# Kernel tuning notes

Measured on AMD Instinct MI355X. Metric: run time of the kernel, lower is better.

Reference implementation:

```python
import jax, jax.numpy as jnp
import numpy as np

EPS = 1e-12
FINAL_GROUPS = 256  # 4*64
FINAL_BIAS = 8.0


def resilu(x):
    # ReSiLU at default hardness == soft sigmoid gate
    return jax.nn.sigmoid(x)


def popcnt_layer(x, sel, w, b):
    # x: [B, In], sel: [O, P] int, w: [O, P], b: [O]
    selected = jnp.take(x, sel, axis=1)          # [B, O, P] gather
    weighted = selected * resilu(w)[None, :, :]  # weighted multiply
    summed = weighted.sum(axis=-1)               # [B, O] segment sum
    return resilu(summed - b[None, :])


def layer_norm(x, g, b):
    mu = x.mean(axis=-1, keepdims=True)
    var = ((x - mu) ** 2).mean(axis=-1, keepdims=True)
    return (x - mu) * jax.lax.rsqrt(var + EPS) * g + b


def setup_inputs() -> dict:
    key = jax.random.key(0)
    ks = jax.random.split(key, 16)
    B, IN, O1, O3, P = 256, 3200, 8192, 4096, 128
    return {
        "x": jax.random.normal(ks[0], (B, IN), dtype=jnp.float32),
        "sel1": jax.random.randint(ks[1], (O1, P), 0, IN, dtype=jnp.int32),
        "w1": jax.random.normal(ks[2], (O1, P), dtype=jnp.float32),
        "b1": jax.random.normal(ks[3], (O1,), dtype=jnp.float32) * (P / 3) + (P / 4),
        "g1": jnp.ones((O1,), dtype=jnp.float32),
        "be1": jnp.zeros((O1,), dtype=jnp.float32),
        "sel2": jax.random.randint(ks[4], (O1, P), 0, O1, dtype=jnp.int32),
        "w2": jax.random.normal(ks[5], (O1, P), dtype=jnp.float32),
        "b2": jax.random.normal(ks[6], (O1,), dtype=jnp.float32) * (P / 3) + (P / 4),
        "g2": jnp.ones((O1,), dtype=jnp.float32),
        "be2": jnp.zeros((O1,), dtype=jnp.float32),
        "sel3": jax.random.randint(ks[7], (O3, P), 0, O1, dtype=jnp.int32),
        "w3": jax.random.normal(ks[8], (O3, P), dtype=jnp.float32),
        "b3": jax.random.normal(ks[9], (O3,), dtype=jnp.float32) * (P / 3) + (P / 4),
    }


def reference(x, sel1, w1, b1, g1, be1, sel2, w2, b2, g2, be2, sel3, w3, b3):
    h = popcnt_layer(x, sel1, w1, b1)
    h = layer_norm(h, g1, be1)
    h = popcnt_layer(h, sel2, w2, b2)
    h = layer_norm(h, g2, be2)
    h = popcnt_layer(h, sel3, w3, b3)          # [B, 4096]
    out = h.reshape(h.shape[0], FINAL_GROUPS, -1).sum(axis=-1) - FINAL_BIAS  # [B, 256]
    return out
```

## Files before the change

kernel.cpp:

```cpp
#include <hip/hip_runtime.h>
#include <hip/hip_fp16.h>
#include <stdint.h>

#define BATCH 256
#define PSEL  128
#define IN_DIM 3200
#define O1_DIM 8192
#define O3_DIM 4096

__global__ __launch_bounds__(256) void transpose_kernel(const float* __restrict__ x,
                                                        __half* __restrict__ xT,
                                                        float* __restrict__ stats) {
    int tx = threadIdx.x;
    int ty = threadIdx.y;
    int tid = ty * 32 + tx;
    int gid = blockIdx.y * gridDim.x + blockIdx.x;
    if (gid < 4) stats[gid * 256 + tid] = 0.0f;

    __shared__ float tile[32][33];
    int i0 = blockIdx.x * 32;
    int b0 = blockIdx.y * 32;
#pragma unroll
    for (int k = 0; k < 4; ++k)
        tile[ty + k * 8][tx] =
            __builtin_nontemporal_load(&x[(size_t)(b0 + ty + k * 8) * IN_DIM + i0 + tx]);
    __syncthreads();
#pragma unroll
    for (int k = 0; k < 4; ++k)
        xT[(size_t)(i0 + ty + k * 8) * BATCH + b0 + tx] =
            __float2half(tile[tx][ty + k * 8]);
}

__global__ __launch_bounds__(256) void stats_kernel(const __half* __restrict__ hT,
                                                    float* __restrict__ gsum,
                                                    float* __restrict__ gsq) {
    int t   = threadIdx.x;
    int col = t & 127;
    int rp  = t >> 7;
    int r0  = blockIdx.x * 128 + rp * 64;
    const uint32_t* p = (const uint32_t*)hT + (size_t)r0 * 128 + col;
    float s0 = 0.f, s1 = 0.f, q0 = 0.f, q1 = 0.f;
#pragma unroll
    for (int ob = 0; ob < 8; ++ob) {
        uint32_t d[8];
#pragma unroll
        for (int j = 0; j < 8; ++j) d[j] = p[(size_t)(ob * 8 + j) * 128];
#pragma unroll
        for (int j = 0; j < 8; ++j) {
            float2 f = __half22float2(*(const __half2*)&d[j]);
            s0 += f.x; q0 = fmaf(f.x, f.x, q0);
            s1 += f.y; q1 = fmaf(f.y, f.y, q1);
        }
    }
    __shared__ float4 s_red[128];
    if (rp == 1) s_red[col] = make_float4(s0, s1, q0, q1);
    __syncthreads();
    if (rp == 0) {
        float4 r = s_red[col];
        atomicAdd(&gsum[2 * col],     s0 + r.x);
        atomicAdd(&gsum[2 * col + 1], s1 + r.y);
        atomicAdd(&gsq[2 * col],      q0 + r.z);
        atomicAdd(&gsq[2 * col + 1],  q1 + r.w);
    }
}

template <bool NORM>
__global__ __launch_bounds__(256, 4) void popcnt_kernel(
    const __half* __restrict__ actT,
    const int* __restrict__ sel,
    const float* __restrict__ w,
    const float* __restrict__ bias,
    const float* __restrict__ g,
    const float* __restrict__ be,
    const float* __restrict__ gsum,
    const float* __restrict__ gsq,
    float inv_n,
    __half* __restrict__ outp)
{
    const int o  = blockIdx.x;
    const int t  = threadIdx.x;
    const int cw = t & 31;
    const int rg = t >> 5;

    __shared__ uint32_t s_off[PSEL];
    __shared__ float    s_A[PSEL];
    __shared__ float s_rA[PSEL], s_rC[PSEL];
    __shared__ float s_acc[8][264];
    __shared__ float s_sums[2];

    if (t < PSEL) {
        int idx  = __builtin_nontemporal_load(&sel[o * PSEL + t]);
        float ww = __builtin_nontemporal_load(&w[o * PSEL + t]);
        float sw = 1.0f / (1.0f + __expf(-ww));
        float a, c;
        if (NORM) { a = sw * g[idx]; c = sw * be[idx]; }
        else      { a = sw;          c = 0.0f; }
        s_off[t] = (uint32_t)idx << 9;
        s_A[t]   = a;
        if (NORM) { s_rA[t] = a; s_rC[t] = c; }
    }
    __syncthreads();

    if (NORM && t < 64) {
        float va = s_rA[t] + s_rA[t + 64];
        float vc = s_rC[t] + s_rC[t + 64];
#pragma unroll
        for (int off = 32; off > 0; off >>= 1) {
            va += __shfl_down(va, off, 64);
            vc += __shfl_down(vc, off, 64);
        }
        if (t == 0) { s_sums[0] = va; s_sums[1] = vc; }
    }

    const uint32_t lane_off = (uint32_t)(cw << 4);
    uint32_t voff[16];
#pragma unroll
    for (int j = 0; j < 16; ++j)
        voff[j] = s_off[j * 8 + rg] + lane_off;
    uint4 d[16];
#pragma unroll
    for (int j = 0; j < 16; ++j)
        asm volatile("global_load_dwordx4 %0, %1, %2 sc0"
                     : "=v"(d[j])
                     : "v"(voff[j]), "s"(actT)
                     : "memory");
    asm volatile("s_waitcnt vmcnt(0)" ::: "memory");
    __builtin_amdgcn_sched_barrier(0);

    float acc[8] = {0.f, 0.f, 0.f, 0.f, 0.f, 0.f, 0.f, 0.f};
#pragma unroll
    for (int j = 0; j < 16; ++j) {
        float A = s_A[j * 8 + rg];
        const __half2* hp = (const __half2*)&d[j];
        float2 f0 = __half22float2(hp[0]);
        float2 f1 = __half22float2(hp[1]);
        float2 f2 = __half22float2(hp[2]);
        float2 f3 = __half22float2(hp[3]);
        acc[0] = fmaf(A, f0.x, acc[0]);
        acc[1] = fmaf(A, f0.y, acc[1]);
        acc[2] = fmaf(A, f1.x, acc[2]);
        acc[3] = fmaf(A, f1.y, acc[3]);
        acc[4] = fmaf(A, f2.x, acc[4]);
        acc[5] = fmaf(A, f2.y, acc[5]);
        acc[6] = fmaf(A, f3.x, acc[6]);
        acc[7] = fmaf(A, f3.y, acc[7]);
    }

    *(float4*)&s_acc[rg][8 * cw]     = make_float4(acc[0], acc[1], acc[2], acc[3]);
    *(float4*)&s_acc[rg][8 * cw + 4] = make_float4(acc[4], acc[5], acc[6], acc[7]);
    __syncthreads();

    float ab = 0.0f;
#pragma unroll
    for (int r = 0; r < 8; ++r) ab += s_acc[r][t];

    float bo = bias[o];
    float z;
    if (NORM) {
        float m  = gsum[t] * inv_n;
        float q  = gsq[t] * inv_n;
        float rs = rsqrtf(q - m * m + 1e-12f);
        z = rs * ab + s_sums[1] - rs * m * s_sums[0] - bo;
    } else {
        z = ab - bo;
    }
    float h = 1.0f / (1.0f + __expf(-z));
    __builtin_nontemporal_store(__half_as_ushort(__float2half(h)),
                                (unsigned short*)outp + (size_t)o * BATCH + t);
}

__global__ __launch_bounds__(256) void final_reduce(const __half* __restrict__ h3T,
                                                    float* __restrict__ out) {
    int gidx = blockIdx.x;
    int b    = threadIdx.x;
    const unsigned short* p = (const unsigned short*)h3T + (size_t)gidx * 16 * BATCH + b;
    float s = -8.0f;
#pragma unroll
    for (int j = 0; j < 16; ++j)
        s += __half2float(__ushort_as_half(__builtin_nontemporal_load(p + j * BATCH)));
    __builtin_nontemporal_store(s, &out[(size_t)b * 256 + gidx]);
}

extern "C" void kernel_launch(void* const* d_in, const int* in_sizes, int n_in,
                              void* d_out, int out_size, void* d_ws, size_t ws_size,
                              hipStream_t stream) {
    const float* x    = (const float*)d_in[0];
    const int*   sel1 = (const int*)d_in[1];
    const float* w1   = (const float*)d_in[2];
    const float* b1   = (const float*)d_in[3];
    const float* g1   = (const float*)d_in[4];
    const float* be1  = (const float*)d_in[5];
    const int*   sel2 = (const int*)d_in[6];
    const float* w2   = (const float*)d_in[7];
    const float* b2   = (const float*)d_in[8];
    const float* g2   = (const float*)d_in[9];
    const float* be2  = (const float*)d_in[10];
    const int*   sel3 = (const int*)d_in[11];
    const float* w3   = (const float*)d_in[12];
    const float* b3   = (const float*)d_in[13];
    float* out = (float*)d_out;

    char* ws = (char*)d_ws;
    __half* xT  = (__half*)(ws);
    __half* h1T = (__half*)(ws + 1638400);
    __half* h2T = (__half*)(ws + 1638400 + 4194304);
    __half* h3T = h1T;
    float* stats = (float*)(ws + 1638400 + 2 * 4194304);
    float* gs1 = stats;
    float* gq1 = stats + 256;
    float* gs2 = stats + 512;
    float* gq2 = stats + 768;

    transpose_kernel<<<dim3(IN_DIM / 32, BATCH / 32), dim3(32, 8), 0, stream>>>(
        x, xT, stats);

    popcnt_kernel<false><<<O1_DIM, 256, 0, stream>>>(
        xT, sel1, w1, b1, nullptr, nullptr, nullptr, nullptr, 0.0f, h1T);

    stats_kernel<<<O1_DIM / 128, 256, 0, stream>>>(h1T, gs1, gq1);

    popcnt_kernel<true><<<O1_DIM, 256, 0, stream>>>(
        h1T, sel2, w2, b2, g1, be1, gs1, gq1, 1.0f / (float)O1_DIM, h2T);

    stats_kernel<<<O1_DIM / 128, 256, 0, stream>>>(h2T, gs2, gq2);

    popcnt_kernel<true><<<O3_DIM, 256, 0, stream>>>(
        h2T, sel3, w3, b3, g2, be2, gs2, gq2, 1.0f / (float)O1_DIM, h3T);

    final_reduce<<<256, 256, 0, stream>>>(h3T, out);
}
```

Before: 181.6 us.

## Process several outputs per block with software-pipelined gather prefetch

Each popcnt block now handles 8 (or 4) consecutive outputs instead of one. The gather loads, sel and w for the next output are issued while the current output is reduced and stored, using double-buffered shared offsets and weights. Per-batch normalization factors are computed once per block. This aims to hide gather latency and cut per-block launch and setup overhead, but grid parallelism drops and the hand-written waitcnt counts make the schedule fragile.

```diff
diff --git a/kernel.cpp b/kernel.cpp
--- a/kernel.cpp
+++ b/kernel.cpp
@@ -75,98 +75,171 @@
     const float* __restrict__ gsum,
     const float* __restrict__ gsq,
     float inv_n,
-    __half* __restrict__ outp)
+    __half* __restrict__ outp,
+    int nout)
 {
-    const int o  = blockIdx.x;
     const int t  = threadIdx.x;
     const int cw = t & 31;
     const int rg = t >> 5;
-
-    __shared__ uint32_t s_off[PSEL];
-    __shared__ float    s_A[PSEL];
-    __shared__ float s_rA[PSEL], s_rC[PSEL];
-    __shared__ float s_acc[8][264];
-    __shared__ float s_sums[2];
+    const int o0 = blockIdx.x * nout;
+
+    __shared__ uint32_t s_off[2][PSEL];
+    __shared__ float    s_A[2][PSEL];
+    __shared__ float    s_part[2][4];
+    __shared__ float    s_acc[8][264];
+
+    const uint32_t lane_off = (uint32_t)(cw << 4);
+
+    float rs = 0.0f, rsm = 0.0f;
+    if (NORM) {
+        float m = gsum[t] * inv_n;
+        float q = gsq[t] * inv_n;
+        rs  = rsqrtf(q - m * m + 1e-12f);
+        rsm = rs * m;
+    }
 
     if (t < PSEL) {
-        int idx  = __builtin_nontemporal_load(&sel[o * PSEL + t]);
-        float ww = __builtin_nontemporal_load(&w[o * PSEL + t]);
-        float sw = 1.0f / (1.0f + __expf(-ww));
+        int   sv = sel[(size_t)o0 * PSEL + t];
+        float wv = w[(size_t)o0 * PSEL + t];
+        float sw = 1.0f / (1.0f + __expf(-wv));
         float a, c;
-        if (NORM) { a = sw * g[idx]; c = sw * be[idx]; }
-        else      { a = sw;          c = 0.0f; }
-        s_off[t] = (uint32_t)idx << 9;
-        s_A[t]   = a;
-        if (NORM) { s_rA[t] = a; s_rC[t] = c; }
+        if (NORM) { a = sw * g[sv]; c = sw * be[sv]; }
+        else      { a = sw;         c = 0.0f; }
+        s_off[0][t] = (uint32_t)sv << 9;
+        s_A[0][t]   = a;
+        if (NORM) {
+            float va = a, vc = c;
+#pragma unroll
+            for (int off = 32; off > 0; off >>= 1) {
+                va += __shfl_down(va, off, 64);
+                vc += __shfl_down(vc, off, 64);
+            }
+            if ((t & 63) == 0) {
+                s_part[0][(t >> 6) * 2 + 0] = va;
+                s_part[0][(t >> 6) * 2 + 1] = vc;
+            }
+        }
     }
     __syncthreads();
 
-    if (NORM && t < 64) {
-        float va = s_rA[t] + s_rA[t + 64];
-        float vc = s_rC[t] + s_rC[t + 64];
-#pragma unroll
-        for (int off = 32; off > 0; off >>= 1) {
-            va += __shfl_down(va, off, 64);
-            vc += __shfl_down(vc, off, 64);
-        }
-        if (t == 0) { s_sums[0] = va; s_sums[1] = vc; }
-    }
-
-    const uint32_t lane_off = (uint32_t)(cw << 4);
-    uint32_t voff[16];
-#pragma unroll
-    for (int j = 0; j < 16; ++j)
-        voff[j] = s_off[j * 8 + rg] + lane_off;
+    uint32_t raw_sel = 0, raw_w = 0;
+    if (nout > 1 && t < PSEL) {
+        const int*   sp = sel + (size_t)(o0 + 1) * PSEL;
+        const float* wp = w   + (size_t)(o0 + 1) * PSEL;
+        uint32_t vo = (uint32_t)(t * 4);
+        asm volatile("global_load_dword %0, %1, %2 nt" : "=v"(raw_sel) : "v"(vo), "s"(sp) : "memory");
+        asm volatile("global_load_dword %0, %1, %2 nt" : "=v"(raw_w)   : "v"(vo), "s"(wp) : "memory");
+    }
     uint4 d[16];
-#pragma unroll
-    for (int j = 0; j < 16; ++j)
-        asm volatile("global_load_dwordx4 %0, %1, %2 sc0"
-                     : "=v"(d[j])
-                     : "v"(voff[j]), "s"(actT)
-                     : "memory");
-    asm volatile("s_waitcnt vmcnt(0)" ::: "memory");
-    __builtin_amdgcn_sched_barrier(0);
-
-    float acc[8] = {0.f, 0.f, 0.f, 0.f, 0.f, 0.f, 0.f, 0.f};
-#pragma unroll
-    for (int j = 0; j < 16; ++j) {
-        float A = s_A[j * 8 + rg];
-        const __half2* hp = (const __half2*)&d[j];
-        float2 f0 = __half22float2(hp[0]);
-        float2 f1 = __half22float2(hp[1]);
-        float2 f2 = __half22float2(hp[2]);
-        float2 f3 = __half22float2(hp[3]);
-        acc[0] = fmaf(A, f0.x, acc[0]);
-        acc[1] = fmaf(A, f0.y, acc[1]);
-        acc[2] = fmaf(A, f1.x, acc[2]);
-        acc[3] = fmaf(A, f1.y, acc[3]);
-        acc[4] = fmaf(A, f2.x, acc[4]);
-        acc[5] = fmaf(A, f2.y, acc[5]);
-        acc[6] = fmaf(A, f3.x, acc[6]);
-        acc[7] = fmaf(A, f3.y, acc[7]);
-    }
-
-    *(float4*)&s_acc[rg][8 * cw]     = make_float4(acc[0], acc[1], acc[2], acc[3]);
-    *(float4*)&s_acc[rg][8 * cw + 4] = make_float4(acc[4], acc[5], acc[6], acc[7]);
-    __syncthreads();
-
-    float ab = 0.0f;
-#pragma unroll
-    for (int r = 0; r < 8; ++r) ab += s_acc[r][t];
-
-    float bo = bias[o];
-    float z;
-    if (NORM) {
-        float m  = gsum[t] * inv_n;
-        float q  = gsq[t] * inv_n;
-        float rs = rsqrtf(q - m * m + 1e-12f);
-        z = rs * ab + s_sums[1] - rs * m * s_sums[0] - bo;
-    } else {
-        z = ab - bo;
-    }
-    float h = 1.0f / (1.0f + __expf(-z));
-    __builtin_nontemporal_store(__half_as_ushort(__float2half(h)),
-                                (unsigned short*)outp + (size_t)o * BATCH + t);
+    {
+        uint32_t voff[16];
+#pragma unroll
+        for (int j = 0; j < 16; ++j) voff[j] = s_off[0][j * 8 + rg] + lane_off;
+#pragma unroll
+        for (int j = 0; j < 16; ++j)
+            asm volatile("global_load_dwordx4 %0, %1, %2 sc0"
+                         : "=v"(d[j]) : "v"(voff[j]), "s"(actT) : "memory");
+    }
+
+    for (int i = 0; i < nout; ++i) {
+        const int cur = i & 1, nxt = cur ^ 1;
+        const bool havenext = (i + 1 < nout);
+
+        float sw_n = 0.0f; int sv_n = 0;
+        uint32_t gv_u = 0, bv_u = 0;
+        if (havenext && t < PSEL) {
+            asm volatile("s_waitcnt vmcnt(16)" ::: "memory");
+            __builtin_amdgcn_sched_barrier(0);
+            sv_n = (int)raw_sel;
+            float wv = __uint_as_float(raw_w);
+            sw_n = 1.0f / (1.0f + __expf(-wv));
+            if (NORM) {
+                uint32_t vo = (uint32_t)(sv_n * 4);
+                asm volatile("global_load_dword %0, %1, %2" : "=v"(gv_u) : "v"(vo), "s"(g)  : "memory");
+                asm volatile("global_load_dword %0, %1, %2" : "=v"(bv_u) : "v"(vo), "s"(be) : "memory");
+            }
+        }
+
+        asm volatile("s_waitcnt vmcnt(0)" ::: "memory");
+        __builtin_amdgcn_sched_barrier(0);
+        if (havenext && t < PSEL) {
+            float a, c;
+            if (NORM) { a = sw_n * __uint_as_float(gv_u); c = sw_n * __uint_as_float(bv_u); }
+            else      { a = sw_n;                         c = 0.0f; }
+            s_off[nxt][t] = (uint32_t)sv_n << 9;
+            s_A[nxt][t]   = a;
+            if (NORM) {
+                float va = a, vc = c;
+#pragma unroll
+                for (int off = 32; off > 0; off >>= 1) {
+                    va += __shfl_down(va, off, 64);
+                    vc += __shfl_down(vc, off, 64);
+                }
+                if ((t & 63) == 0) {
+                    s_part[nxt][(t >> 6) * 2 + 0] = va;
+                    s_part[nxt][(t >> 6) * 2 + 1] = vc;
+                }
+            }
+        }
+        float acc[8] = {0.f, 0.f, 0.f, 0.f, 0.f, 0.f, 0.f, 0.f};
+#pragma unroll
+        for (int j = 0; j < 16; ++j) {
+            float A = s_A[cur][j * 8 + rg];
+            const __half2* hp = (const __half2*)&d[j];
+            float2 f0 = __half22float2(hp[0]);
+            float2 f1 = __half22float2(hp[1]);
+            float2 f2 = __half22float2(hp[2]);
+            float2 f3 = __half22float2(hp[3]);
+            acc[0] = fmaf(A, f0.x, acc[0]);
+            acc[1] = fmaf(A, f0.y, acc[1]);
+            acc[2] = fmaf(A, f1.x, acc[2]);
+            acc[3] = fmaf(A, f1.y, acc[3]);
+            acc[4] = fmaf(A, f2.x, acc[4]);
+            acc[5] = fmaf(A, f2.y, acc[5]);
+            acc[6] = fmaf(A, f3.x, acc[6]);
+            acc[7] = fmaf(A, f3.y, acc[7]);
+        }
+        *(float4*)&s_acc[rg][8 * cw]     = make_float4(acc[0], acc[1], acc[2], acc[3]);
+        *(float4*)&s_acc[rg][8 * cw + 4] = make_float4(acc[4], acc[5], acc[6], acc[7]);
+        asm volatile("s_waitcnt lgkmcnt(0)" ::: "memory");
+        __builtin_amdgcn_s_barrier();
+
+        if (i + 2 < nout && t < PSEL) {
+            const int*   sp = sel + (size_t)(o0 + i + 2) * PSEL;
+            const float* wp = w   + (size_t)(o0 + i + 2) * PSEL;
+            uint32_t vo = (uint32_t)(t * 4);
+            asm volatile("global_load_dword %0, %1, %2 nt" : "=v"(raw_sel) : "v"(vo), "s"(sp) : "memory");
+            asm volatile("global_load_dword %0, %1, %2 nt" : "=v"(raw_w)   : "v"(vo), "s"(wp) : "memory");
+        }
+        if (havenext) {
+            uint32_t voff[16];
+#pragma unroll
+            for (int j = 0; j < 16; ++j) voff[j] = s_off[nxt][j * 8 + rg] + lane_off;
+#pragma unroll
+            for (int j = 0; j < 16; ++j)
+                asm volatile("global_load_dwordx4 %0, %1, %2 sc0"
+                             : "=v"(d[j]) : "v"(voff[j]), "s"(actT) : "memory");
+        }
+
+        float ab = 0.0f;
+#pragma unroll
+        for (int r = 0; r < 8; ++r) ab += s_acc[r][t];
+        float bo = bias[o0 + i];
+        float z;
+        if (NORM) {
+            float sA = s_part[cur][0] + s_part[cur][2];
+            float sC = s_part[cur][1] + s_part[cur][3];
+            z = rs * ab + sC - rsm * sA - bo;
+        } else {
+            z = ab - bo;
+        }
+        float h = 1.0f / (1.0f + __expf(-z));
+        __builtin_nontemporal_store(__half_as_ushort(__float2half(h)),
+                                    (unsigned short*)outp + (size_t)(o0 + i) * BATCH + t);
+
+        asm volatile("s_waitcnt lgkmcnt(0)" ::: "memory");
+        __builtin_amdgcn_s_barrier();
+    }
 }
 
 __global__ __launch_bounds__(256) void final_reduce(const __half* __restrict__ h3T,
@@ -214,18 +287,18 @@
     transpose_kernel<<<dim3(IN_DIM / 32, BATCH / 32), dim3(32, 8), 0, stream>>>(
         x, xT, stats);
 
-    popcnt_kernel<false><<<O1_DIM, 256, 0, stream>>>(
-        xT, sel1, w1, b1, nullptr, nullptr, nullptr, nullptr, 0.0f, h1T);
+    popcnt_kernel<false><<<O1_DIM / 8, 256, 0, stream>>>(
+        xT, sel1, w1, b1, nullptr, nullptr, nullptr, nullptr, 0.0f, h1T, 8);
 
     stats_kernel<<<O1_DIM / 128, 256, 0, stream>>>(h1T, gs1, gq1);
 
-    popcnt_kernel<true><<<O1_DIM, 256, 0, stream>>>(
-        h1T, sel2, w2, b2, g1, be1, gs1, gq1, 1.0f / (float)O1_DIM, h2T);
+    popcnt_kernel<true><<<O1_DIM / 8, 256, 0, stream>>>(
+        h1T, sel2, w2, b2, g1, be1, gs1, gq1, 1.0f / (float)O1_DIM, h2T, 8);
 
     stats_kernel<<<O1_DIM / 128, 256, 0, stream>>>(h2T, gs2, gq2);
 
-    popcnt_kernel<true><<<O3_DIM, 256, 0, stream>>>(
-        h2T, sel3, w3, b3, g2, be2, gs2, gq2, 1.0f / (float)O1_DIM, h3T);
+    popcnt_kernel<true><<<O3_DIM / 4, 256, 0, stream>>>(
+        h2T, sel3, w3, b3, g2, be2, gs2, gq2, 1.0f / (float)O1_DIM, h3T, 4);
 
     final_reduce<<<256, 256, 0, stream>>>(h3T, out);
 }
```

After: 191.8 us. 1.06x slower.

## Fuse final popcnt layer with group-sum reduction via atomics, prefetch next params

Applied to the files above, without the earlier changes.

Folds the last popcnt layer and the final group reduction into one kernel. Each block handles 4 outputs and atomically adds sigmoid results into an output buffer that the transpose kernel pre-initialises to the final bias. The next output's selection and weight parameters are loaded while the current gathers are in flight. It also halves the stats kernel grid by giving each block twice as many rows. This removes one kernel launch and the h3 round trip, at the cost of float atomics (non-deterministic summation order) and fewer blocks in the last layer.

```diff
diff --git a/kernel.cpp b/kernel.cpp
--- a/kernel.cpp
+++ b/kernel.cpp
@@ -10,12 +10,14 @@
 
 __global__ __launch_bounds__(256) void transpose_kernel(const float* __restrict__ x,
                                                         __half* __restrict__ xT,
+                                                        float* __restrict__ out,
                                                         float* __restrict__ stats) {
     int tx = threadIdx.x;
     int ty = threadIdx.y;
     int tid = ty * 32 + tx;
     int gid = blockIdx.y * gridDim.x + blockIdx.x;
-    if (gid < 4) stats[gid * 256 + tid] = 0.0f;
+    if (gid < 256) out[gid * 256 + tid] = -8.0f;
+    else if (gid < 260) stats[(gid - 256) * 256 + tid] = 0.0f;
 
     __shared__ float tile[32][33];
     int i0 = blockIdx.x * 32;
@@ -37,11 +39,11 @@
     int t   = threadIdx.x;
     int col = t & 127;
     int rp  = t >> 7;
-    int r0  = blockIdx.x * 128 + rp * 64;
+    int r0  = blockIdx.x * 256 + rp * 128;
     const uint32_t* p = (const uint32_t*)hT + (size_t)r0 * 128 + col;
     float s0 = 0.f, s1 = 0.f, q0 = 0.f, q1 = 0.f;
 #pragma unroll
-    for (int ob = 0; ob < 8; ++ob) {
+    for (int ob = 0; ob < 16; ++ob) {
         uint32_t d[8];
 #pragma unroll
         for (int j = 0; j < 8; ++j) d[j] = p[(size_t)(ob * 8 + j) * 128];
@@ -169,16 +171,125 @@
                                 (unsigned short*)outp + (size_t)o * BATCH + t);
 }
 
-__global__ __launch_bounds__(256) void final_reduce(const __half* __restrict__ h3T,
-                                                    float* __restrict__ out) {
-    int gidx = blockIdx.x;
-    int b    = threadIdx.x;
-    const unsigned short* p = (const unsigned short*)h3T + (size_t)gidx * 16 * BATCH + b;
-    float s = -8.0f;
-#pragma unroll
-    for (int j = 0; j < 16; ++j)
-        s += __half2float(__ushort_as_half(__builtin_nontemporal_load(p + j * BATCH)));
-    __builtin_nontemporal_store(s, &out[(size_t)b * 256 + gidx]);
+template <int NOUT>
+__global__ __launch_bounds__(256, 4) void popcnt_final_kernel(
+    const __half* __restrict__ actT,
+    const int* __restrict__ sel,
+    const float* __restrict__ w,
+    const float* __restrict__ bias,
+    const float* __restrict__ g,
+    const float* __restrict__ be,
+    const float* __restrict__ gsum,
+    const float* __restrict__ gsq,
+    float inv_n,
+    float* __restrict__ out)
+{
+    const int t  = threadIdx.x;
+    const int cw = t & 31;
+    const int rg = t >> 5;
+    const int o0 = blockIdx.x * NOUT;
+
+    __shared__ uint32_t s_off[2][PSEL];
+    __shared__ float    s_A[2][PSEL];
+    __shared__ float    s_part[2][4];
+    __shared__ float    s_acc[8][264];
+
+    const uint32_t lane_off = (uint32_t)(cw << 4);
+
+    float m  = gsum[t] * inv_n;
+    float q  = gsq[t] * inv_n;
+    float rs = rsqrtf(q - m * m + 1e-12f);
+    float rsm = rs * m;
+
+    if (t < PSEL) {
+        int   sv = sel[(size_t)o0 * PSEL + t];
+        float wv = w[(size_t)o0 * PSEL + t];
+        float sw = 1.0f / (1.0f + __expf(-wv));
+        float a = sw * g[sv], c = sw * be[sv];
+        s_off[0][t] = (uint32_t)sv << 9;
+        s_A[0][t]   = a;
+        float va = a, vc = c;
+#pragma unroll
+        for (int off = 32; off > 0; off >>= 1) {
+            va += __shfl_down(va, off, 64);
+            vc += __shfl_down(vc, off, 64);
+        }
+        if ((t & 63) == 0) {
+            s_part[0][(t >> 6) * 2 + 0] = va;
+            s_part[0][(t >> 6) * 2 + 1] = vc;
+        }
+    }
+    __syncthreads();
+
+#pragma unroll
+    for (int i = 0; i < NOUT; ++i) {
+        const int cur = i & 1, nxt = cur ^ 1;
+
+        uint32_t voff[16];
+#pragma unroll
+        for (int j = 0; j < 16; ++j) voff[j] = s_off[cur][j * 8 + rg] + lane_off;
+        uint4 d[16];
+#pragma unroll
+        for (int j = 0; j < 16; ++j)
+            asm volatile("global_load_dwordx4 %0, %1, %2 sc0"
+                         : "=v"(d[j]) : "v"(voff[j]), "s"(actT) : "memory");
+
+        if (i + 1 < NOUT && t < PSEL) {
+            int   sv = sel[(size_t)(o0 + i + 1) * PSEL + t];
+            float wv = w[(size_t)(o0 + i + 1) * PSEL + t];
+            float sw = 1.0f / (1.0f + __expf(-wv));
+            float a = sw * g[sv], c = sw * be[sv];
+            s_off[nxt][t] = (uint32_t)sv << 9;
+            s_A[nxt][t]   = a;
+            float va = a, vc = c;
+#pragma unroll
+            for (int off = 32; off > 0; off >>= 1) {
+                va += __shfl_down(va, off, 64);
+                vc += __shfl_down(vc, off, 64);
+            }
+            if ((t & 63) == 0) {
+                s_part[nxt][(t >> 6) * 2 + 0] = va;
+                s_part[nxt][(t >> 6) * 2 + 1] = vc;
+            }
+        }
+
+        asm volatile("s_waitcnt vmcnt(0)" ::: "memory");
+        __builtin_amdgcn_sched_barrier(0);
+
+        float acc[8] = {0.f, 0.f, 0.f, 0.f, 0.f, 0.f, 0.f, 0.f};
+#pragma unroll
+        for (int j = 0; j < 16; ++j) {
+            float A = s_A[cur][j * 8 + rg];
+            const __half2* hp = (const __half2*)&d[j];
+            float2 f0 = __half22float2(hp[0]);
+            float2 f1 = __half22float2(hp[1]);
+            float2 f2 = __half22float2(hp[2]);
+            float2 f3 = __half22float2(hp[3]);
+            acc[0] = fmaf(A, f0.x, acc[0]);
+            acc[1] = fmaf(A, f0.y, acc[1]);
+            acc[2] = fmaf(A, f1.x, acc[2]);
+            acc[3] = fmaf(A, f1.y, acc[3]);
+            acc[4] = fmaf(A, f2.x, acc[4]);
+            acc[5] = fmaf(A, f2.y, acc[5]);
+            acc[6] = fmaf(A, f3.x, acc[6]);
+            acc[7] = fmaf(A, f3.y, acc[7]);
+        }
+        *(float4*)&s_acc[rg][8 * cw]     = make_float4(acc[0], acc[1], acc[2], acc[3]);
+        *(float4*)&s_acc[rg][8 * cw + 4] = make_float4(acc[4], acc[5], acc[6], acc[7]);
+        __syncthreads();
+
+        float ab = 0.0f;
+#pragma unroll
+        for (int r = 0; r < 8; ++r) ab += s_acc[r][t];
+        float bo = bias[o0 + i];
+        float sA = s_part[cur][0] + s_part[cur][2];
+        float sC = s_part[cur][1] + s_part[cur][3];
+        float z = rs * ab + sC - rsm * sA - bo;
+        float h = 1.0f / (1.0f + __expf(-z));
+        atomicAdd(&out[(size_t)t * 256 + ((o0 + i) >> 4)], h);
+
+        __syncthreads();
+    }
 }
 
 extern "C" void kernel_launch(void* const* d_in, const int* in_sizes, int n_in,
@@ -204,7 +315,6 @@
     __half* xT  = (__half*)(ws);
     __half* h1T = (__half*)(ws + 1638400);
     __half* h2T = (__half*)(ws + 1638400 + 4194304);
-    __half* h3T = h1T;
     float* stats = (float*)(ws + 1638400 + 2 * 4194304);
     float* gs1 = stats;
     float* gq1 = stats + 256;
@@ -212,20 +322,18 @@
     float* gq2 = stats + 768;
 
     transpose_kernel<<<dim3(IN_DIM / 32, BATCH / 32), dim3(32, 8), 0, stream>>>(
-        x, xT, stats);
+        x, xT, out, stats);
 
     popcnt_kernel<false><<<O1_DIM, 256, 0, stream>>>(
         xT, sel1, w1, b1, nullptr, nullptr, nullptr, nullptr, 0.0f, h1T);
 
-    stats_kernel<<<O1_DIM / 128, 256, 0, stream>>>(h1T, gs1, gq1);
+    stats_kernel<<<O1_DIM / 256, 256, 0, stream>>>(h1T, gs1, gq1);
 
     popcnt_kernel<true><<<O1_DIM, 256, 0, stream>>>(
         h1T, sel2, w2, b2, g1, be1, gs1, gq1, 1.0f / (float)O1_DIM, h2T);
 
-    stats_kernel<<<O1_DIM / 128, 256, 0, stream>>>(h2T, gs2, gq2);
-
-    popcnt_kernel<true><<<O3_DIM, 256, 0, stream>>>(
-        h2T, sel3, w3, b3, g2, be2, gs2, gq2, 1.0f / (float)O1_DIM, h3T);
-
-    final_reduce<<<256, 256, 0, stream>>>(h3T, out);
-}
+    stats_kernel<<<O1_DIM / 256, 256, 0, stream>>>(h2T, gs2, gq2);
+
+    popcnt_final_kernel<4><<<O3_DIM / 4, 256, 0, stream>>>(
+        h2T, sel3, w3, b3, g2, be2, gs2, gq2, 1.0f / (float)O1_DIM, out);
+}
```

Result: slower. 215.6 us (+18.7%).
